# Kernel tuning notes

Hardware: AMD Instinct MI355X
Metric: run time of the kernel (lower is better)

## Reference

```python
import jax, jax.numpy as jnp
import numpy as np

B, S, D, H, E, K = 2, 2048, 1024, 4096, 8, 2


def setup_inputs() -> dict:
    key = jax.random.key(0)
    ks = jax.random.split(key, 7)
    sd = 1.0 / np.sqrt(D)
    sh = 1.0 / np.sqrt(H)
    return {
        "x": jax.random.normal(ks[0], (B, S, D), dtype=jnp.float32),
        "Wr": jax.random.uniform(ks[1], (D, E), jnp.float32, -sd, sd),
        "br": jnp.zeros((E,), jnp.float32),
        "W1": jax.random.uniform(ks[2], (E, D, H), jnp.float32, -sd, sd),
        "b1": jax.random.uniform(ks[3], (E, H), jnp.float32, -sd, sd),
        "W2": jax.random.uniform(ks[4], (E, H, D), jnp.float32, -sh, sh),
        "b2": jax.random.uniform(ks[5], (E, D), jnp.float32, -sh, sh),
    }


def reference(x, Wr, br, W1, b1, W2, b2):
    # Router
    router_logits = jnp.einsum("bsd,de->bse", x, Wr) + br          # [B,S,E]
    topk_logits, topk_idx = jax.lax.top_k(router_logits, K)          # [B,S,K]
    gates = jax.nn.softmax(topk_logits, axis=-1)                     # [B,S,K]

    # Dense all-expert FFN (math identical to masked per-expert GEMMs)
    h = jax.nn.gelu(jnp.einsum("bsd,edh->ebsh", x, W1) + b1[:, None, None, :],
                    approximate=False)                                # [E,B,S,H]
    y = jnp.einsum("ebsh,ehd->bsed", h, W2) + b2[None, None, :, :]    # [B,S,E,D]

    # Gather the top-k experts per token and combine with gates
    sel = jnp.take_along_axis(y, topk_idx[..., None], axis=2)         # [B,S,K,D]
    out = jnp.sum(gates[..., None] * sel, axis=2)                     # [B,S,D]

    # Load-balancing aux loss
    probs = jax.nn.softmax(router_logits, axis=-1)
    importance = probs.mean(axis=(0, 1))                              # [E]
    aux_loss = jnp.mean((importance - 1.0 / E) ** 2)
    return out, aux_loss
```

## Files before the change

kernel.cpp:

```cpp
#include <hip/hip_runtime.h>
#include <hip/hip_bf16.h>
#include <math.h>

#define NTOK 4096
#define DD   1024
#define HH   4096
#define EE   8
#define NSLOT 8192
#define NSLOT_PAD 8320
#define RBLK 128

typedef __bf16 bf16x8 __attribute__((ext_vector_type(8)));
typedef float  f32x4  __attribute__((ext_vector_type(4)));

#define WS_COUNTS     0
#define WS_CURSORS    64
#define WS_OFFSETS    128
#define WS_IMP        256
#define WS_TOPK_IDX   512
#define WS_TOPK_GATE  33280
#define WS_SLOT_OF    66048
#define WS_TOKEN_LIST 98816
#define WS_XG         131584
#define WS_HBUF       17170944
#define WS_YBUF       85328384
#define WS_W1BT       118882816
#define WS_W2BT       185991680
#define WS_CNT_PART   (WS_HBUF + (size_t)NSLOT * HH * 2)
#define WS_IMP_PART   (WS_HBUF + (size_t)NSLOT * HH * 2 + 4096)

__device__ __forceinline__ float gelu_exact(float v) {
    return 0.5f * v * (1.0f + erff(v * 0.70710678118654752f));
}

__device__ __forceinline__ void async_copy16(const __bf16* g, __bf16* l) {
    __builtin_amdgcn_global_load_lds(
        (const __attribute__((address_space(1))) void*)g,
        (__attribute__((address_space(3))) void*)l, 16, 0, 0);
}

__launch_bounds__(256)
__global__ void router_kernel(const float* __restrict__ x,
                              const float* __restrict__ Wr,
                              const float* __restrict__ br,
                              int* __restrict__ cntPart,
                              float* __restrict__ impPart,
                              int* __restrict__ topk_idx,
                              float* __restrict__ topk_gate) {
    __shared__ float WrL[DD * EE];
    __shared__ float impW[4][EE];
    __shared__ int cntL[EE];
    int tid = threadIdx.x;
    int lane = tid & 63, wave = tid >> 6;
    int grp = lane >> 3, e = lane & 7;
    int t = blockIdx.x * 32 + wave * 8 + grp;

    for (int i = tid; i < DD * EE / 4; i += 256)
        ((float4*)WrL)[i] = ((const float4*)Wr)[i];
    if (tid < EE) cntL[tid] = 0;
    __syncthreads();

    const float* xr = x + (size_t)t * DD;
    float acc = 0.f;
#pragma unroll 4
    for (int d = 0; d < DD; d += 4) {
        float4 xv = *(const float4*)(xr + d);
        acc = fmaf(xv.x, WrL[(d + 0) * EE + e], acc);
        acc = fmaf(xv.y, WrL[(d + 1) * EE + e], acc);
        acc = fmaf(xv.z, WrL[(d + 2) * EE + e], acc);
        acc = fmaf(xv.w, WrL[(d + 3) * EE + e], acc);
    }
    float l = acc + br[e];

    float m = l;
#pragma unroll
    for (int mk = 1; mk <= 4; mk <<= 1) m = fmaxf(m, __shfl_xor(m, mk, 64));
    float p = expf(l - m);
    float s = p;
#pragma unroll
    for (int mk = 1; mk <= 4; mk <<= 1) s += __shfl_xor(s, mk, 64);
    p /= s;

    float bl = l; int be = e;
#pragma unroll
    for (int mk = 1; mk <= 4; mk <<= 1) {
        float ol = __shfl_xor(bl, mk, 64);
        int   oe = __shfl_xor(be, mk, 64);
        if (ol > bl || (ol == bl && oe < be)) { bl = ol; be = oe; }
    }
    int e1 = be; float l1 = bl;
    float cl = (e == e1) ? -INFINITY : l; int ce = e;
#pragma unroll
    for (int mk = 1; mk <= 4; mk <<= 1) {
        float ol = __shfl_xor(cl, mk, 64);
        int   oe = __shfl_xor(ce, mk, 64);
        if (ol > cl || (ol == cl && oe < ce)) { cl = ol; ce = oe; }
    }
    int e2 = ce; float l2 = cl;

    if (e == 0) {
        float bb = expf(l2 - l1);
        float g1 = 1.f / (1.f + bb);
        topk_idx[t * 2 + 0] = e1; topk_idx[t * 2 + 1] = e2;
        topk_gate[t * 2 + 0] = g1; topk_gate[t * 2 + 1] = bb * g1;
        atomicAdd(&cntL[e1], 1);
        atomicAdd(&cntL[e2], 1);
    }

#pragma unroll
    for (int mk = 8; mk <= 32; mk <<= 1) p += __shfl_xor(p, mk, 64);
    if (lane < 8) impW[wave][lane] = p;
    __syncthreads();
    if (tid < EE) {
        float v = impW[0][tid] + impW[1][tid] + impW[2][tid] + impW[3][tid];
        impPart[blockIdx.x * EE + tid] = v;
        cntPart[blockIdx.x * EE + tid] = cntL[tid];
    }
}

__launch_bounds__(64)
__global__ void prefix_kernel(const int* __restrict__ cntPart,
                              const float* __restrict__ impPart,
                              int* __restrict__ offsets,
                              int* __restrict__ cursors,
                              float* __restrict__ aux_out) {
    __shared__ int cs[EE];
    __shared__ float is[EE];
    int tid = threadIdx.x;
    if (tid < EE) {
        int c = 0; float v = 0.f;
        for (int b = 0; b < RBLK; b++) {
            c += cntPart[b * EE + tid];
            v += impPart[b * EE + tid];
        }
        cs[tid] = c; is[tid] = v;
    }
    __syncthreads();
    if (tid == 0) {
        int o = 0;
        for (int e = 0; e < EE; e++) { offsets[e] = o; cursors[e] = o; o += cs[e]; }
        offsets[EE] = o;
        float aux = 0.f;
        for (int e = 0; e < EE; e++) {
            float d = is[e] / (float)NTOK - 1.0f / (float)EE;
            aux += d * d;
        }
        aux_out[0] = aux / (float)EE;
    }
}

__launch_bounds__(256)
__global__ void scatter_kernel(const int* __restrict__ topk_idx,
                               int* __restrict__ cursors,
                               int* __restrict__ token_list,
                               int* __restrict__ slot_of) {
    __shared__ int lcnt[EE];
    __shared__ int lbase[EE];
    int tid = threadIdx.x;
    int t = blockIdx.x * 256 + tid;
    if (tid < EE) lcnt[tid] = 0;
    __syncthreads();
    int e0 = topk_idx[t * 2 + 0], e1 = topk_idx[t * 2 + 1];
    int r0 = atomicAdd(&lcnt[e0], 1);
    int r1 = atomicAdd(&lcnt[e1], 1);
    __syncthreads();
    if (tid < EE) lbase[tid] = atomicAdd(&cursors[tid], lcnt[tid]);
    __syncthreads();
    int s0 = lbase[e0] + r0, s1 = lbase[e1] + r1;
    token_list[s0] = t; token_list[s1] = t;
    slot_of[t * 2 + 0] = s0; slot_of[t * 2 + 1] = s1;
}

__launch_bounds__(256)
__global__ void gather_x_kernel(const float* __restrict__ x,
                                const int* __restrict__ token_list,
                                __bf16* __restrict__ xg) {
    int s = blockIdx.x;
    int t = token_list[s];
    int tid = threadIdx.x;
    float4 v = ((const float4*)(x + (size_t)t * DD))[tid];
    __bf16 tmp[4] __attribute__((aligned(8)));
    tmp[0] = (__bf16)v.x; tmp[1] = (__bf16)v.y;
    tmp[2] = (__bf16)v.z; tmp[3] = (__bf16)v.w;
    ((ushort4*)(xg + (size_t)s * DD))[tid] = *(ushort4*)tmp;
}

__launch_bounds__(256)
__global__ void transpose_w_kernel(const float* __restrict__ in,
                                   __bf16* __restrict__ out,
                                   int R, int C) {
    int e = blockIdx.z;
    int c0 = blockIdx.x * 64, r0 = blockIdx.y * 64;
    __shared__ float tile[64][65];
    int tid = threadIdx.x;
    const float* ip = in + (size_t)e * R * C;
#pragma unroll
    for (int i = 0; i < 4; i++) {
        int flat = i * 256 + tid;
        int r = flat >> 4, c4 = (flat & 15) * 4;
        float4 v = *(const float4*)(ip + (size_t)(r0 + r) * C + c0 + c4);
        tile[r][c4 + 0] = v.x; tile[r][c4 + 1] = v.y;
        tile[r][c4 + 2] = v.z; tile[r][c4 + 3] = v.w;
    }
    __syncthreads();
    __bf16* op = out + (size_t)e * C * R;
#pragma unroll
    for (int i = 0; i < 4; i++) {
        int flat = i * 256 + tid;
        int c = flat >> 4, r4 = (flat & 15) * 4;
        __bf16 tmp[4] __attribute__((aligned(8)));
        tmp[0] = (__bf16)tile[r4 + 0][c];
        tmp[1] = (__bf16)tile[r4 + 1][c];
        tmp[2] = (__bf16)tile[r4 + 2][c];
        tmp[3] = (__bf16)tile[r4 + 3][c];
        *(ushort4*)(op + (size_t)(c0 + c) * R + r0 + r4) = *(ushort4*)tmp;
    }
}

template <int N, int K, bool GELU, typename OutT>
__launch_bounds__(256)
__global__ void gemm_bt_kernel(const __bf16* __restrict__ A,
                               const __bf16* __restrict__ Bt,
                               const float* __restrict__ bias,
                               const int* __restrict__ offsets,
                               OutT* __restrict__ Out) {
    int e = blockIdx.z, ct = blockIdx.x, rt = blockIdx.y;
    int obase = offsets[e], cnt = offsets[e + 1] - obase;
    int m0 = rt * 128;
    if (m0 >= cnt) return;

    __shared__ __bf16 As[128 * 64];
    __shared__ __bf16 Bs[128 * 64];

    int tid = threadIdx.x, lane = tid & 63, wave = tid >> 6;
    int quad = lane >> 4, m16 = lane & 15;
    int wm = wave & 1, wn = wave >> 1;
    int srow = lane >> 3;
    int scol = (lane & 7) * 8;

    const __bf16* Ag = A + (size_t)(obase + m0) * K;
    const __bf16* Bg = Bt + ((size_t)e * N + (size_t)ct * 128) * K;

    f32x4 acc[4][4] = {};

    for (int k0 = 0; k0 < K; k0 += 64) {
#pragma unroll
        for (int r = 0; r < 4; r++) {
            int chunk = r * 4 + wave;
            int row = chunk * 8 + srow;
            async_copy16(Ag + (size_t)row * K + k0 + scol, As + chunk * 512);
        }
#pragma unroll
        for (int r = 0; r < 4; r++) {
            int chunk = r * 4 + wave;
            int row = chunk * 8 + srow;
            async_copy16(Bg + (size_t)row * K + k0 + scol, Bs + chunk * 512);
        }
        __syncthreads();
#pragma unroll
        for (int kk = 0; kk < 64; kk += 32) {
            bf16x8 af[4], bfr[4];
#pragma unroll
            for (int mi = 0; mi < 4; mi++)
                af[mi] = *(const bf16x8*)(As + (wm * 64 + mi * 16 + m16) * 64 + kk + quad * 8);
#pragma unroll
            for (int ni = 0; ni < 4; ni++)
                bfr[ni] = *(const bf16x8*)(Bs + (wn * 64 + ni * 16 + m16) * 64 + kk + quad * 8);
#pragma unroll
            for (int mi = 0; mi < 4; mi++)
#pragma unroll
                for (int ni = 0; ni < 4; ni++)
                    acc[mi][ni] = __builtin_amdgcn_mfma_f32_16x16x32_bf16(
                        af[mi], bfr[ni], acc[mi][ni], 0, 0, 0);
        }
        __syncthreads();
    }

    float bv[4];
#pragma unroll
    for (int ni = 0; ni < 4; ni++)
        bv[ni] = bias[(size_t)e * N + ct * 128 + wn * 64 + ni * 16 + m16];
#pragma unroll
    for (int mi = 0; mi < 4; mi++) {
#pragma unroll
        for (int r = 0; r < 4; r++) {
            int row = wm * 64 + mi * 16 + quad * 4 + r;
            if (m0 + row < cnt) {
                size_t orow = (size_t)(obase + m0 + row) * N + (size_t)ct * 128 + wn * 64;
#pragma unroll
                for (int ni = 0; ni < 4; ni++) {
                    float v = acc[mi][ni][r] + bv[ni];
                    if (GELU) v = gelu_exact(v);
                    Out[orow + ni * 16 + m16] = (OutT)v;
                }
            }
        }
    }
}

__launch_bounds__(256)
__global__ void combine_kernel(const float* __restrict__ ybuf,
                               const int* __restrict__ slot_of,
                               const float* __restrict__ topk_gate,
                               float* __restrict__ out) {
    int t = blockIdx.x;
    int tid = threadIdx.x;
    int s0 = slot_of[t * 2 + 0], s1 = slot_of[t * 2 + 1];
    float g0 = topk_gate[t * 2 + 0], g1 = topk_gate[t * 2 + 1];
    const float4* y0 = (const float4*)(ybuf + (size_t)s0 * DD);
    const float4* y1 = (const float4*)(ybuf + (size_t)s1 * DD);
    float4 a = y0[tid], b = y1[tid];
    float4 o;
    o.x = g0 * a.x + g1 * b.x;
    o.y = g0 * a.y + g1 * b.y;
    o.z = g0 * a.z + g1 * b.z;
    o.w = g0 * a.w + g1 * b.w;
    ((float4*)(out + (size_t)t * DD))[tid] = o;
}

extern "C" void kernel_launch(void* const* d_in, const int* in_sizes, int n_in,
                              void* d_out, int out_size, void* d_ws, size_t ws_size,
                              hipStream_t stream) {
    const float* x  = (const float*)d_in[0];
    const float* Wr = (const float*)d_in[1];
    const float* br = (const float*)d_in[2];
    const float* W1 = (const float*)d_in[3];
    const float* b1 = (const float*)d_in[4];
    const float* W2 = (const float*)d_in[5];
    const float* b2 = (const float*)d_in[6];
    float* out = (float*)d_out;

    char* ws = (char*)d_ws;
    int*    offsets    = (int*)(ws + WS_OFFSETS);
    int*    cursors    = (int*)(ws + WS_CURSORS);
    int*    topk_idx   = (int*)(ws + WS_TOPK_IDX);
    float*  topk_gate  = (float*)(ws + WS_TOPK_GATE);
    int*    slot_of    = (int*)(ws + WS_SLOT_OF);
    int*    token_list = (int*)(ws + WS_TOKEN_LIST);
    __bf16* xg         = (__bf16*)(ws + WS_XG);
    __bf16* hbuf       = (__bf16*)(ws + WS_HBUF);
    float*  ybuf       = (float*)(ws + WS_YBUF);
    __bf16* W1bt       = (__bf16*)(ws + WS_W1BT);
    __bf16* W2bt       = (__bf16*)(ws + WS_W2BT);
    int*    cntPart    = (int*)(ws + WS_CNT_PART);
    float*  impPart    = (float*)(ws + WS_IMP_PART);

    router_kernel<<<RBLK, 256, 0, stream>>>(x, Wr, br, cntPart, impPart, topk_idx, topk_gate);
    prefix_kernel<<<1, 64, 0, stream>>>(cntPart, impPart, offsets, cursors, out + (size_t)NTOK * DD);
    scatter_kernel<<<NTOK / 256, 256, 0, stream>>>(topk_idx, cursors, token_list, slot_of);
    gather_x_kernel<<<NSLOT, 256, 0, stream>>>(x, token_list, xg);

    transpose_w_kernel<<<dim3(HH / 64, DD / 64, EE), 256, 0, stream>>>(W1, W1bt, DD, HH);
    transpose_w_kernel<<<dim3(DD / 64, HH / 64, EE), 256, 0, stream>>>(W2, W2bt, HH, DD);

    gemm_bt_kernel<HH, DD, true, __bf16>
        <<<dim3(HH / 128, NSLOT / 128, EE), 256, 0, stream>>>(xg, W1bt, b1, offsets, hbuf);
    gemm_bt_kernel<DD, HH, false, float>
        <<<dim3(DD / 128, NSLOT / 128, EE), 256, 0, stream>>>(hbuf, W2bt, b2, offsets, ybuf);

    combine_kernel<<<NTOK, 256, 0, stream>>>(ybuf, slot_of, topk_gate, out);
}
```

Baseline: 713.0 us.

## Double-buffer GEMM LDS tiles with async prefetch and XOR swizzle

The expert GEMM kernel now keeps two LDS buffers and issues the async global-to-LDS copies for the next K tile before computing on the current one. It waits on vmcnt so that only the older batch of copies has to finish, which overlaps load latency with MFMA work. LDS reads and writes use an XOR swizzle on the 16-byte column chunk to reduce bank conflicts, and launch bounds now ask for 2 blocks per CU. The weight transpose kernel also switches to 16-byte stores. Risks include doubled LDS use, which may limit occupancy, and correctness that depends on the hand-written waitcnt count.

New measurement: 656.6 us. 1.09x faster.

```diff
diff --git a/kernel.cpp b/kernel.cpp
--- a/kernel.cpp
+++ b/kernel.cpp
@@ -12,6 +12,9 @@
 
 typedef __bf16 bf16x8 __attribute__((ext_vector_type(8)));
 typedef float  f32x4  __attribute__((ext_vector_type(4)));
+typedef unsigned short u16x8 __attribute__((ext_vector_type(8)));
+
+#define WAITCNT_VM(n) (((n) & 0xF) | (0x7 << 4) | (0xF << 8) | (((n) >> 4) << 14))
 
 #define WS_COUNTS     0
 #define WS_CURSORS    64
@@ -205,20 +208,18 @@
     __syncthreads();
     __bf16* op = out + (size_t)e * C * R;
 #pragma unroll
-    for (int i = 0; i < 4; i++) {
+    for (int i = 0; i < 2; i++) {
         int flat = i * 256 + tid;
-        int c = flat >> 4, r4 = (flat & 15) * 4;
-        __bf16 tmp[4] __attribute__((aligned(8)));
-        tmp[0] = (__bf16)tile[r4 + 0][c];
-        tmp[1] = (__bf16)tile[r4 + 1][c];
-        tmp[2] = (__bf16)tile[r4 + 2][c];
-        tmp[3] = (__bf16)tile[r4 + 3][c];
-        *(ushort4*)(op + (size_t)(c0 + c) * R + r0 + r4) = *(ushort4*)tmp;
+        int c = flat >> 3, r8 = (flat & 7) * 8;
+        __bf16 tmp[8] __attribute__((aligned(16)));
+#pragma unroll
+        for (int j = 0; j < 8; j++) tmp[j] = (__bf16)tile[r8 + j][c];
+        *(u16x8*)(op + (size_t)(c0 + c) * R + r0 + r8) = *(u16x8*)tmp;
     }
 }
 
 template <int N, int K, bool GELU, typename OutT>
-__launch_bounds__(256)
+__launch_bounds__(256, 2)
 __global__ void gemm_bt_kernel(const __bf16* __restrict__ A,
                                const __bf16* __restrict__ Bt,
                                const float* __restrict__ bias,
@@ -229,52 +230,77 @@
     int m0 = rt * 128;
     if (m0 >= cnt) return;
 
-    __shared__ __bf16 As[128 * 64];
-    __shared__ __bf16 Bs[128 * 64];
+    __shared__ __bf16 As[2][128 * 64];
+    __shared__ __bf16 Bs[2][128 * 64];
 
     int tid = threadIdx.x, lane = tid & 63, wave = tid >> 6;
     int quad = lane >> 4, m16 = lane & 15;
     int wm = wave & 1, wn = wave >> 1;
     int srow = lane >> 3;
-    int scol = (lane & 7) * 8;
+    int scol = ((lane & 7) ^ srow) * 8;
+    int swz = m16 & 7;
 
     const __bf16* Ag = A + (size_t)(obase + m0) * K;
     const __bf16* Bg = Bt + ((size_t)e * N + (size_t)ct * 128) * K;
 
     f32x4 acc[4][4] = {};
 
-    for (int k0 = 0; k0 < K; k0 += 64) {
-#pragma unroll
-        for (int r = 0; r < 4; r++) {
-            int chunk = r * 4 + wave;
-            int row = chunk * 8 + srow;
-            async_copy16(Ag + (size_t)row * K + k0 + scol, As + chunk * 512);
-        }
-#pragma unroll
-        for (int r = 0; r < 4; r++) {
-            int chunk = r * 4 + wave;
-            int row = chunk * 8 + srow;
-            async_copy16(Bg + (size_t)row * K + k0 + scol, Bs + chunk * 512);
-        }
-        __syncthreads();
-#pragma unroll
-        for (int kk = 0; kk < 64; kk += 32) {
-            bf16x8 af[4], bfr[4];
-#pragma unroll
-            for (int mi = 0; mi < 4; mi++)
-                af[mi] = *(const bf16x8*)(As + (wm * 64 + mi * 16 + m16) * 64 + kk + quad * 8);
-#pragma unroll
-            for (int ni = 0; ni < 4; ni++)
-                bfr[ni] = *(const bf16x8*)(Bs + (wn * 64 + ni * 16 + m16) * 64 + kk + quad * 8);
-#pragma unroll
-            for (int mi = 0; mi < 4; mi++)
-#pragma unroll
-                for (int ni = 0; ni < 4; ni++)
-                    acc[mi][ni] = __builtin_amdgcn_mfma_f32_16x16x32_bf16(
-                        af[mi], bfr[ni], acc[mi][ni], 0, 0, 0);
-        }
-        __syncthreads();
-    }
+#define STAGE(buf, k0)                                                        \
+    {                                                                         \
+        _Pragma("unroll")                                                     \
+        for (int r = 0; r < 4; r++) {                                         \
+            int chunk = r * 4 + wave;                       \
+            int row = chunk * 8 + srow;                                       \
+            async_copy16(Ag + (size_t)row * K + (k0) + scol, As[buf] + chunk * 512); \
+        }                                                                     \
+        _Pragma("unroll")                                                     \
+        for (int r = 0; r < 4; r++) {                                         \
+            int chunk = r * 4 + wave;                                         \
+            int row = chunk * 8 + srow;                                       \
+            async_copy16(Bg + (size_t)row * K + (k0) + scol, Bs[buf] + chunk * 512); \
+        }                                                                     \
+    }
+
+#define COMPUTE(buf)                                                          \
+    {                                                                         \
+        const __bf16* Ac = As[buf];                                           \
+        const __bf16* Bc = Bs[buf];                                           \
+        _Pragma("unroll")                                                     \
+        for (int kk = 0; kk < 64; kk += 32) {                                 \
+            int kkc = kk >> 3;                                                \
+            bf16x8 af[4], bfr[4];                                             \
+            _Pragma("unroll")                                                 \
+            for (int mi = 0; mi < 4; mi++)                                    \
+                af[mi] = *(const bf16x8*)(Ac + (wm * 64 + mi * 16 + m16) * 64 \
+                                          + (((kkc + quad) ^ swz) * 8));      \
+            _Pragma("unroll")                                                 \
+            for (int ni = 0; ni < 4; ni++)                                    \
+                bfr[ni] = *(const bf16x8*)(Bc + (wn * 64 + ni * 16 + m16) * 64\
+                                           + (((kkc + quad) ^ swz) * 8));     \
+            _Pragma("unroll")                                                 \
+            for (int mi = 0; mi < 4; mi++)                                    \
+                _Pragma("unroll")                                             \
+                for (int ni = 0; ni < 4; ni++)                                \
+                    acc[mi][ni] = __builtin_amdgcn_mfma_f32_16x16x32_bf16(    \
+                        af[mi], bfr[ni], acc[mi][ni], 0, 0, 0);               \
+        }                                                                     \
+    }
+
+    STAGE(0, 0);
+    int cur = 0;
+    for (int k0 = 64; k0 < K; k0 += 64) {
+        STAGE(cur ^ 1, k0);
+        __builtin_amdgcn_s_waitcnt(WAITCNT_VM(8));
+        __builtin_amdgcn_s_barrier();
+        COMPUTE(cur);
+        __builtin_amdgcn_s_barrier();
+        cur ^= 1;
+    }
+    __builtin_amdgcn_s_waitcnt(WAITCNT_VM(0));
+    __builtin_amdgcn_s_barrier();
+    COMPUTE(cur);
+#undef STAGE
+#undef COMPUTE
 
     float bv[4];
 #pragma unroll
```
